# Kernel tuning notes

Measured on AMD Instinct MI355X. Metric: run time of the kernel, lower is better.

Reference implementation:

```python
import jax, jax.numpy as jnp
import numpy as np

# dims: n=batch, T=n_shifts, dX=16, dU=8, H=256 hidden, L=128 ldim, K=64 n_aux (L=2K)

def setup_inputs() -> dict:
    key = jax.random.key(0)
    ks = jax.random.split(key, 16)
    n, T, dX, dU, H, L, K = 64, 64, 16, 8, 256, 128, 64
    def lin(k, fan_in, shape):
        return (jax.random.uniform(k, shape, jnp.float32) * 2.0 - 1.0) / np.sqrt(fan_in)
    xs = jax.random.normal(ks[0], (n, T, dX), jnp.float32)
    us = jax.random.normal(ks[1], (n, T - 1, dU), jnp.float32)
    theta = jax.random.uniform(ks[2], (K,), jnp.float32) * (2.0 * np.pi)
    inp = {
        'xs': xs, 'us': us,
        # stacked x-aux encoders (K copies): BN affine, 3 linear layers (last no bias), output scale
        'x_gamma': jnp.ones((K, dX)), 'x_beta': jnp.zeros((K, dX)),
        'xW1': lin(ks[3], dX, (K, dX, H)), 'xb1': jnp.zeros((K, H)),
        'xW2': lin(ks[4], H, (K, H, H)), 'xb2': jnp.zeros((K, H)),
        'xW3': lin(ks[5], H, (K, H, L)), 'x_scale': jnp.ones((K, L)),
        # stacked u-aux encoders (K copies)
        'u_gamma': jnp.ones((K, dU)), 'u_beta': jnp.zeros((K, dU)),
        'uW1': lin(ks[6], dU, (K, dU, H)), 'ub1': jnp.zeros((K, H)),
        'uW2': lin(ks[7], H, (K, H, H)), 'ub2': jnp.zeros((K, H)),
        'uW3': lin(ks[8], H, (K, H, L)), 'u_scale': jnp.ones((K, L)),
        # Jordan-block complex eigenvalues (|lam| ~ 0.95)
        'reL': 0.95 * jnp.cos(theta), 'imL': 0.95 * jnp.sin(theta),
        # decoder C: Linear(ldim, dim, bias=False) -> weight [dX, L]
        'C_W': lin(ks[9], L, (dX, L)),
    }
    return inp


def _encoder(x, gamma, beta, W1, b1, W2, b2, W3, scale):
    # x: [M, D]; stacked params over K nets. BN stats (training mode) are per-feature over M,
    # identical across nets since the same x feeds every net.
    mu = x.mean(0)
    var = ((x - mu) ** 2).mean(0)
    xn = (x - mu) * jax.lax.rsqrt(var + 1e-5)          # [M, D]
    h = xn[None] * gamma[:, None, :] + beta[:, None, :]  # [K, M, D]
    h = jax.nn.leaky_relu(jnp.einsum('kmd,kdh->kmh', h, W1) + b1[:, None, :])
    h = jax.nn.leaky_relu(jnp.einsum('kmd,kdh->kmh', h, W2) + b2[:, None, :])
    h = jnp.einsum('kmd,kdh->kmh', h, W3)               # last layer: no bias
    return h * scale[:, None, :]                        # [K, M, L]


def reference(xs, us, x_gamma, x_beta, xW1, xb1, xW2, xb2, xW3, x_scale,
              u_gamma, u_beta, uW1, ub1, uW2, ub2, uW3, u_scale, reL, imL, C_W):
    n, T, dX = xs.shape
    K = reL.shape[0]
    L = 2 * K
    Tm1 = T - 1
    # phi1s: [n, T, K(net), K(pair), 2]
    phi = _encoder(xs.reshape(n * T, dX), x_gamma, x_beta, xW1, xb1, xW2, xb2, xW3, x_scale)
    phi1s = jnp.moveaxis(phi, 0, 1).reshape(n, T, K, K, 2)
    # ures = psi(u) - psi(0): [n, T-1, K, K, 2]
    uflat = us.reshape(n * Tm1, -1)
    psi_u = _encoder(uflat, u_gamma, u_beta, uW1, ub1, uW2, ub2, uW3, u_scale)
    psi_0 = _encoder(jnp.zeros_like(uflat), u_gamma, u_beta, uW1, ub1, uW2, ub2, uW3, u_scale)
    ures = jnp.moveaxis(psi_u - psi_0, 0, 1).reshape(n, Tm1, K, K, 2)
    # block-diagonal Koopman: per net j a 2x2 rotation-scale [[re, im], [-im, re]]
    R = jnp.stack([jnp.stack([reL, imL], -1), jnp.stack([-imL, reL], -1)], -2)  # [K, 2, 2]

    def step(p, u_t):
        p = jnp.einsum('bjkc,jcd->bjkd', p + u_t, R)
        return p, p

    _, preds = jax.lax.scan(step, phi1s[:, 0], jnp.moveaxis(ures, 0, 1))
    preds = jnp.moveaxis(preds, 0, 1)  # [n, T-1, K, K, 2]

    def phi2y(p):
        # sum over net axis (-3), flatten pair dims -> [.., L], decode with C
        return p.sum(-3).reshape(*p.shape[:-3], L) @ C_W.T

    y = phi2y(phi1s[:, 1:])
    y_pred = phi2y(preds)
    return y, y_pred
```

## Files before the change

### kernel.cpp

```cpp
#include <hip/hip_runtime.h>

typedef __bf16 bf16_t;
typedef __bf16 bf16x8 __attribute__((ext_vector_type(8)));
typedef __bf16 bf16x4 __attribute__((ext_vector_type(4)));
typedef float  f32x4  __attribute__((ext_vector_type(4)));

__global__ __launch_bounds__(256) void bn_partial_kernel(
    const float* __restrict__ xs, const float* __restrict__ us,
    float* __restrict__ part) {
    const int bid = blockIdx.x, tid = threadIdx.x;
    const bool isx = bid < 64;
    const float* x = isx ? xs : us;
    const int D   = isx ? 16 : 8;
    const int lb  = isx ? bid : bid - 64;
    const int per = isx ? (4096 * 16 / 64) : (4032 * 8 / 32);
    const int start = lb * per;
    float a = 0.f, b = 0.f;
    for (int idx = start + tid; idx < start + per; idx += 256) {
        float v = x[idx];
        a += v; b += v * v;
    }
    __shared__ float s1[256], s2[256];
    s1[tid] = a; s2[tid] = b;
    __syncthreads();
    if (tid < D) {
        float sa = 0.f, sb = 0.f;
        for (int k = tid; k < 256; k += D) { sa += s1[k]; sb += s2[k]; }
        part[bid * 32 + tid]      = sa;
        part[bid * 32 + 16 + tid] = sb;
    }
}

__global__ __launch_bounds__(64) void bn_final_kernel(
    const float* __restrict__ part, float* __restrict__ stats_x, float* __restrict__ stats_u) {
    const int tid = threadIdx.x;
    if (tid < 16) {
        float sa = 0.f, sb = 0.f;
        for (int b = 0; b < 64; b++) { sa += part[b * 32 + tid]; sb += part[b * 32 + 16 + tid]; }
        float mu = sa / 4096.f, var = sb / 4096.f - mu * mu;
        stats_x[tid] = mu; stats_x[16 + tid] = rsqrtf(var + 1e-5f);
    } else if (tid >= 32 && tid < 40) {
        const int d = tid - 32;
        float sa = 0.f, sb = 0.f;
        for (int b = 64; b < 96; b++) { sa += part[b * 32 + d]; sb += part[b * 32 + 16 + d]; }
        float mu = sa / 4032.f, var = sb / 4032.f - mu * mu;
        stats_u[d] = mu; stats_u[8 + d] = rsqrtf(var + 1e-5f);
    }
}

__global__ __launch_bounds__(256) void prep_w1_kernel(
    const float* __restrict__ xW1, const float* __restrict__ xb1,
    const float* __restrict__ xg,  const float* __restrict__ xbeta,
    const float* __restrict__ uW1, const float* __restrict__ ub1,
    const float* __restrict__ ug,  const float* __restrict__ ubeta,
    bf16_t* __restrict__ xW1t, float* __restrict__ xb1p,
    bf16_t* __restrict__ uW1t, float* __restrict__ ub1p) {
    int bid = blockIdx.x, j = bid & 63, h = threadIdx.x;
    const float *W1, *b1, *gamma, *beta; bf16_t* W1t; float* b1p; int D;
    if (bid < 64) { W1 = xW1; b1 = xb1; gamma = xg; beta = xbeta; W1t = xW1t; b1p = xb1p; D = 16; }
    else          { W1 = uW1; b1 = ub1; gamma = ug; beta = ubeta; W1t = uW1t; b1p = ub1p; D = 8; }
    float bacc = b1[j * 256 + h];
    bf16_t* orow = W1t + (size_t)(j * 256 + h) * 32;
    for (int d = 0; d < 32; d++) orow[d] = (bf16_t)0.f;
    for (int d = 0; d < D; d++) {
        float w = W1[((size_t)j * D + d) * 256 + h];
        orow[d] = (bf16_t)(gamma[j * D + d] * w);
        bacc += beta[j * D + d] * w;
    }
    b1p[j * 256 + h] = bacc;
}

__global__ __launch_bounds__(256) void transpose_all_kernel(
    const float* __restrict__ xW2, const float* __restrict__ uW2,
    const float* __restrict__ xW3, const float* __restrict__ uW3,
    const float* __restrict__ x_scale, const float* __restrict__ u_scale,
    bf16_t* __restrict__ xW2t, bf16_t* __restrict__ uW2t,
    bf16_t* __restrict__ xW3t, bf16_t* __restrict__ uW3t) {
    __shared__ float tile[32][33];
    int z = blockIdx.z, b = z & 63;
    const float* in; bf16_t* outp; const float* scale = nullptr; int C;
    if (z < 64)       { in = xW2; outp = xW2t; C = 256; }
    else if (z < 128) { in = uW2; outp = uW2t; C = 256; }
    else if (z < 192) { in = xW3; outp = xW3t; scale = x_scale + b * 128; C = 128; if (blockIdx.x >= 4) return; }
    else              { in = uW3; outp = uW3t; scale = u_scale + b * 128; C = 128; if (blockIdx.x >= 4) return; }
    const int R = 256;
    in   += (size_t)b * R * C;
    outp += (size_t)b * R * C;
    int r0 = blockIdx.y * 32, c0 = blockIdx.x * 32;
    int tx = threadIdx.x & 31, ty = threadIdx.x >> 5;
    #pragma unroll
    for (int i = 0; i < 4; i++)
        tile[ty + i * 8][tx] = in[(size_t)(r0 + ty + i * 8) * C + c0 + tx];
    __syncthreads();
    #pragma unroll
    for (int i = 0; i < 4; i++) {
        int c = c0 + ty + i * 8;
        float sc = scale ? scale[c] : 1.f;
        outp[(size_t)c * R + r0 + tx] = (bf16_t)(tile[tx][ty + i * 8] * sc);
    }
}

__global__ __launch_bounds__(512, 4) void fused_mlp_kernel(
    const float* __restrict__ xs, const float* __restrict__ us,
    const float* __restrict__ stats_x, const float* __restrict__ stats_u,
    const bf16_t* __restrict__ xW1t, const float* __restrict__ xb1p,
    const bf16_t* __restrict__ xW2t, const float* __restrict__ xb2,
    const bf16_t* __restrict__ xW3t,
    const bf16_t* __restrict__ uW1t, const float* __restrict__ ub1p,
    const bf16_t* __restrict__ uW2t, const float* __restrict__ ub2,
    const bf16_t* __restrict__ uW3t,
    bf16_t* __restrict__ phi, bf16_t* __restrict__ psiu)
{
    const int bid  = blockIdx.x;
    const int xcd  = bid & 7;
    const int slot = bid >> 3;
    const int band = slot >> 6;
    const int t64  = slot & 63;
    const int j    = xcd * 8 + band;
    const bool is_x = t64 < 32;
    const int tile  = is_x ? t64 : (t64 - 32);

    const float*  In    = is_x ? xs      : us;
    const float*  stats = is_x ? stats_x : stats_u;
    const int     D     = is_x ? 16      : 8;
    const bf16_t* W1t = is_x ? xW1t : uW1t;
    const float*  b1p = is_x ? xb1p : ub1p;
    const bf16_t* W2t = is_x ? xW2t : uW2t;
    const float*  b2  = is_x ? xb2  : ub2;
    const bf16_t* W3t = is_x ? xW3t : uW3t;
    bf16_t* outp      = is_x ? phi  : psiu;
    const int M       = is_x ? 4096 : 4032;

    const int row0 = tile * 128;
    const int tid  = threadIdx.x;
    const int wave = tid >> 6;
    const int lane = tid & 63;
    const int quad = lane >> 4;
    const int l16  = lane & 15;

    __shared__ __align__(16) bf16_t hs[128 * 256];

    const f32x4 vzero = {0.f, 0.f, 0.f, 0.f};

    {
        bf16x8 wfr[2];
        #pragma unroll
        for (int nbi = 0; nbi < 2; nbi++)
            wfr[nbi] = *reinterpret_cast<const bf16x8*>(
                W1t + (size_t)(j * 256 + wave * 32 + nbi * 16 + l16) * 32 + quad * 8);

        f32x4 acc[8][2];
        #pragma unroll
        for (int a = 0; a < 8; a++) { acc[a][0] = vzero; acc[a][1] = vzero; }

        const int c0 = quad * 8;
        #pragma unroll
        for (int mb = 0; mb < 8; mb++) {
            bf16x8 a;
            if (c0 < D) {
                int row = row0 + mb * 16 + l16;
                if (row > M - 1) row = M - 1;
                const float* xp = In + (size_t)row * D + c0;
                f32x4 v0 = *reinterpret_cast<const f32x4*>(xp);
                f32x4 v1 = *reinterpret_cast<const f32x4*>(xp + 4);
                #pragma unroll
                for (int e = 0; e < 4; e++) a[e]     = (bf16_t)((v0[e] - stats[c0 + e])     * stats[D + c0 + e]);
                #pragma unroll
                for (int e = 0; e < 4; e++) a[4 + e] = (bf16_t)((v1[e] - stats[c0 + 4 + e]) * stats[D + c0 + 4 + e]);
            } else {
                #pragma unroll
                for (int e = 0; e < 8; e++) a[e] = (bf16_t)0.f;
            }
            #pragma unroll
            for (int nbi = 0; nbi < 2; nbi++)
                acc[mb][nbi] = __builtin_amdgcn_mfma_f32_16x16x32_bf16(
                    wfr[nbi], a, acc[mb][nbi], 0, 0, 0);
        }

        #pragma unroll
        for (int nbi = 0; nbi < 2; nbi++) {
            const f32x4 bias = *reinterpret_cast<const f32x4*>(
                b1p + j * 256 + wave * 32 + nbi * 16 + quad * 4);
            const int sl = wave * 4 + nbi * 2 + (quad >> 1);
            const int half = quad & 1;
            const int sp = sl ^ l16;
            #pragma unroll
            for (int mb = 0; mb < 8; mb++) {
                const int m = mb * 16 + l16;
                bf16x4 pk;
                #pragma unroll
                for (int r = 0; r < 4; r++) {
                    float v = acc[mb][nbi][r] + bias[r];
                    v = fmaxf(v, 0.01f * v);
                    pk[r] = (bf16_t)v;
                }
                *reinterpret_cast<bf16x4*>(hs + m * 256 + sp * 8 + half * 4) = pk;
            }
        }
    }
    __syncthreads();

    {
        f32x4 acc[8][2];
        #pragma unroll
        for (int a = 0; a < 8; a++) { acc[a][0] = vzero; acc[a][1] = vzero; }

        const bf16_t* w2base = W2t + ((size_t)j * 256 + wave * 32 + l16) * 256 + quad * 8;

        bf16x8 wr[3][2];
        #pragma unroll
        for (int d = 0; d < 3; d++)
            #pragma unroll
            for (int nbi = 0; nbi < 2; nbi++)
                wr[d][nbi] = *reinterpret_cast<const bf16x8*>(w2base + nbi * 4096 + d * 32);

        #pragma unroll
        for (int kk = 0; kk < 8; kk++) {
            const int c = kk % 3;
            bf16x8 av0[4];
            #pragma unroll
            for (int mb = 0; mb < 4; mb++)
                av0[mb] = *reinterpret_cast<const bf16x8*>(
                    hs + (mb * 16 + l16) * 256 + (((kk * 4 + quad) ^ l16)) * 8);
            #pragma unroll
            for (int nbi = 0; nbi < 2; nbi++)
                #pragma unroll
                for (int mb = 0; mb < 4; mb++)
                    acc[mb][nbi] = __builtin_amdgcn_mfma_f32_16x16x32_bf16(
                        wr[c][nbi], av0[mb], acc[mb][nbi], 0, 0, 0);
            bf16x8 av1[4];
            #pragma unroll
            for (int mb = 4; mb < 8; mb++)
                av1[mb - 4] = *reinterpret_cast<const bf16x8*>(
                    hs + (mb * 16 + l16) * 256 + (((kk * 4 + quad) ^ l16)) * 8);
            #pragma unroll
            for (int nbi = 0; nbi < 2; nbi++)
                #pragma unroll
                for (int mb = 4; mb < 8; mb++)
                    acc[mb][nbi] = __builtin_amdgcn_mfma_f32_16x16x32_bf16(
                        wr[c][nbi], av1[mb - 4], acc[mb][nbi], 0, 0, 0);
            if (kk < 5) {
                #pragma unroll
                for (int nbi = 0; nbi < 2; nbi++)
                    wr[c][nbi] = *reinterpret_cast<const bf16x8*>(
                        w2base + nbi * 4096 + (kk + 3) * 32);
            }
        }
        __syncthreads();
        #pragma unroll
        for (int nbi = 0; nbi < 2; nbi++) {
            const f32x4 bias = *reinterpret_cast<const f32x4*>(
                b2 + j * 256 + wave * 32 + nbi * 16 + quad * 4);
            const int sl = wave * 4 + nbi * 2 + (quad >> 1);
            const int half = quad & 1;
            const int sp = sl ^ l16;
            #pragma unroll
            for (int mb = 0; mb < 8; mb++) {
                const int m = mb * 16 + l16;
                bf16x4 pk;
                #pragma unroll
                for (int r = 0; r < 4; r++) {
                    float v = acc[mb][nbi][r] + bias[r];
                    v = fmaxf(v, 0.01f * v);
                    pk[r] = (bf16_t)v;
                }
                *reinterpret_cast<bf16x4*>(hs + m * 256 + sp * 8 + half * 4) = pk;
            }
        }
    }
    __syncthreads();

    {
        f32x4 acc[8];
        #pragma unroll
        for (int a = 0; a < 8; a++) acc[a] = vzero;

        const bf16_t* w3base = W3t + ((size_t)j * 128 + wave * 16 + l16) * 256 + quad * 8;

        bf16x8 wr[3];
        #pragma unroll
        for (int d = 0; d < 3; d++)
            wr[d] = *reinterpret_cast<const bf16x8*>(w3base + d * 32);

        #pragma unroll
        for (int kk = 0; kk < 8; kk++) {
            const int c = kk % 3;
            bf16x8 av0[4];
            #pragma unroll
            for (int mb = 0; mb < 4; mb++)
                av0[mb] = *reinterpret_cast<const bf16x8*>(
                    hs + (mb * 16 + l16) * 256 + (((kk * 4 + quad) ^ l16)) * 8);
            #pragma unroll
            for (int mb = 0; mb < 4; mb++)
                acc[mb] = __builtin_amdgcn_mfma_f32_16x16x32_bf16(
                    wr[c], av0[mb], acc[mb], 0, 0, 0);
            bf16x8 av1[4];
            #pragma unroll
            for (int mb = 4; mb < 8; mb++)
                av1[mb - 4] = *reinterpret_cast<const bf16x8*>(
                    hs + (mb * 16 + l16) * 256 + (((kk * 4 + quad) ^ l16)) * 8);
            #pragma unroll
            for (int mb = 4; mb < 8; mb++)
                acc[mb] = __builtin_amdgcn_mfma_f32_16x16x32_bf16(
                    wr[c], av1[mb - 4], acc[mb], 0, 0, 0);
            if (kk < 5)
                wr[c] = *reinterpret_cast<const bf16x8*>(w3base + (kk + 3) * 32);
        }
        __syncthreads();
        {
            const int sl3 = wave * 2 + (quad >> 1);
            const int half = quad & 1;
            #pragma unroll
            for (int mb = 0; mb < 8; mb++) {
                const int m = mb * 16 + l16;
                const int sp = sl3 ^ l16;
                bf16x4 pk;
                #pragma unroll
                for (int r = 0; r < 4; r++) pk[r] = (bf16_t)acc[mb][r];
                *reinterpret_cast<bf16x4*>(hs + m * 128 + sp * 8 + half * 4) = pk;
            }
        }
    }
    __syncthreads();
    #pragma unroll
    for (int p = 0; p < 4; p++) {
        const int rr = p * 32 + (tid >> 4);
        const int s  = tid & 15;
        if (row0 + rr < M) {
            bf16x8 v = *reinterpret_cast<const bf16x8*>(hs + rr * 128 + (s ^ (rr & 15)) * 8);
            *reinterpret_cast<bf16x8*>(outp + ((size_t)j * M + row0 + rr) * 128 + s * 8) = v;
        }
    }
}

__global__ __launch_bounds__(256) void psi0_kernel(
    const float* __restrict__ b1p, const bf16_t* __restrict__ W2t,
    const float* __restrict__ b2, const bf16_t* __restrict__ W3t,
    float* __restrict__ psi0) {
    int j = blockIdx.x, tid = threadIdx.x;
    __shared__ float h1[256], h2[256];
    {
        float v = b1p[j * 256 + tid];
        h1[tid] = fmaxf(v, 0.01f * v);
    }
    __syncthreads();
    {
        float acc = b2[j * 256 + tid];
        const bf16_t* wrow = W2t + (size_t)(j * 256 + tid) * 256;
        for (int d = 0; d < 256; d++) acc += h1[d] * (float)wrow[d];
        h2[tid] = fmaxf(acc, 0.01f * acc);
    }
    __syncthreads();
    if (tid < 128) {
        float acc = 0.f;
        const bf16_t* wrow = W3t + (size_t)(j * 128 + tid) * 256;
        for (int d = 0; d < 256; d++) acc += h2[d] * (float)wrow[d];
        psi0[j * 128 + tid] = acc;
    }
}

__global__ __launch_bounds__(256) void y_kernel(
    const bf16_t* __restrict__ phi, const float* __restrict__ C_W,
    float* __restrict__ y) {
    const int m0 = blockIdx.x * 32;
    const int tid = threadIdx.x;
    const int r  = tid >> 3;
    const int cg = (tid & 7) * 16;
    float acc[16];
    #pragma unroll
    for (int e = 0; e < 16; e++) acc[e] = 0.f;
    const bf16_t* p = phi + (size_t)(m0 + r) * 128 + cg;
    for (int j = 0; j < 64; j++) {
        bf16x8 v0 = *reinterpret_cast<const bf16x8*>(p + (size_t)j * 524288);
        bf16x8 v1 = *reinterpret_cast<const bf16x8*>(p + (size_t)j * 524288 + 8);
        #pragma unroll
        for (int e = 0; e < 8; e++) { acc[e] += (float)v0[e]; acc[8 + e] += (float)v1[e]; }
    }
    __shared__ float S[32][128];
    #pragma unroll
    for (int e = 0; e < 16; e++) S[r][cg + e] = acc[e];
    __syncthreads();
    #pragma unroll
    for (int i = 0; i < 2; i++) {
        const int idx = tid + i * 256;
        const int mm = idx >> 4, o = idx & 15;
        const int m = m0 + mm;
        if ((m & 63) != 0) {
            float a = 0.f;
            for (int l = 0; l < 128; l++) a += S[mm][l] * C_W[o * 128 + l];
            const int b = m >> 6, ti = (m & 63) - 1;
            y[(b * 63 + ti) * 16 + o] = a;
        }
    }
}

__global__ __launch_bounds__(256) void scan_kernel(
    const bf16_t* __restrict__ phi, const bf16_t* __restrict__ psiu,
    const float* __restrict__ psi0, const float* __restrict__ reL,
    const float* __restrict__ imL, float* __restrict__ scratch) {
    const int b = blockIdx.x >> 3, jg = blockIdx.x & 7;
    const int tid = threadIdx.x;
    const int wave = tid >> 6, lane = tid & 63;
    __shared__ float red[2][4][128];

    float sx[2], sy[2], p0x[2], p0y[2], lre[2], lim[2];
    #pragma unroll
    for (int i = 0; i < 2; i++) {
        const int j = jg * 8 + wave * 2 + i;
        unsigned v = *reinterpret_cast<const unsigned*>(
            phi + ((size_t)j * 4096 + b * 64) * 128 + lane * 2);
        sx[i] = __uint_as_float(v << 16);
        sy[i] = __uint_as_float(v & 0xFFFF0000u);
        float2 p0 = *reinterpret_cast<const float2*>(psi0 + j * 128 + lane * 2);
        p0x[i] = p0.x; p0y[i] = p0.y;
        lre[i] = reL[j]; lim[i] = imL[j];
    }
    float* out = scratch + (size_t)blockIdx.x * 63 * 128;

    for (int t = 0; t < 63; t++) {
        float lsx = 0.f, lsy = 0.f;
        #pragma unroll
        for (int i = 0; i < 2; i++) {
            const int j = jg * 8 + wave * 2 + i;
            unsigned v = *reinterpret_cast<const unsigned*>(
                psiu + ((size_t)j * 4032 + b * 63 + t) * 128 + lane * 2);
            float px = sx[i] + (__uint_as_float(v << 16) - p0x[i]);
            float py = sy[i] + (__uint_as_float(v & 0xFFFF0000u) - p0y[i]);
            sx[i] = px * lre[i] - py * lim[i];
            sy[i] = px * lim[i] + py * lre[i];
            lsx += sx[i]; lsy += sy[i];
        }
        const int db = t & 1;
        red[db][wave][lane * 2]     = lsx;
        red[db][wave][lane * 2 + 1] = lsy;
        __syncthreads();
        if (tid < 128)
            out[t * 128 + tid] = red[db][0][tid] + red[db][1][tid]
                               + red[db][2][tid] + red[db][3][tid];
    }
}

__global__ __launch_bounds__(64) void decode_kernel(
    const float* __restrict__ scratch, const float* __restrict__ C_W,
    float* __restrict__ ypred) {
    const int t = blockIdx.x, b = blockIdx.y, l = threadIdx.x;
    __shared__ float S[128];
    float s0 = 0.f, s1 = 0.f;
    #pragma unroll
    for (int jg = 0; jg < 8; jg++) {
        float2 v = *reinterpret_cast<const float2*>(
            scratch + ((size_t)(b * 8 + jg) * 63 + t) * 128 + l * 2);
        s0 += v.x; s1 += v.y;
    }
    S[l * 2] = s0; S[l * 2 + 1] = s1;
    __syncthreads();
    const int o = l >> 2, q = l & 3;
    float acc = 0.f;
    #pragma unroll
    for (int i = 0; i < 32; i++)
        acc += S[q * 32 + i] * C_W[o * 128 + q * 32 + i];
    acc += __shfl_xor(acc, 2, 4);
    acc += __shfl_xor(acc, 1, 4);
    if (q == 0) ypred[(b * 63 + t) * 16 + o] = acc;
}

extern "C" void kernel_launch(void* const* d_in, const int* in_sizes, int n_in,
                              void* d_out, int out_size, void* d_ws, size_t ws_size,
                              hipStream_t stream) {
    const float* xs      = (const float*)d_in[0];
    const float* us      = (const float*)d_in[1];
    const float* x_gamma = (const float*)d_in[2];
    const float* x_beta  = (const float*)d_in[3];
    const float* xW1     = (const float*)d_in[4];
    const float* xb1     = (const float*)d_in[5];
    const float* xW2     = (const float*)d_in[6];
    const float* xb2     = (const float*)d_in[7];
    const float* xW3     = (const float*)d_in[8];
    const float* x_scale = (const float*)d_in[9];
    const float* u_gamma = (const float*)d_in[10];
    const float* u_beta  = (const float*)d_in[11];
    const float* uW1     = (const float*)d_in[12];
    const float* ub1     = (const float*)d_in[13];
    const float* uW2     = (const float*)d_in[14];
    const float* ub2     = (const float*)d_in[15];
    const float* uW3     = (const float*)d_in[16];
    const float* u_scale = (const float*)d_in[17];
    const float* reL     = (const float*)d_in[18];
    const float* imL     = (const float*)d_in[19];
    const float* C_W     = (const float*)d_in[20];

    char* ws = (char*)d_ws;
    size_t off = 0;
    auto alloc = [&](size_t bytes) -> char* {
        char* p = ws + off;
        off += (bytes + 255) & ~(size_t)255;
        return p;
    };
    float*  part    = (float*)alloc(96 * 32 * 4);
    float*  stats_x = (float*)alloc(64 * 4);
    float*  stats_u = (float*)alloc(64 * 4);
    bf16_t* xW1t = (bf16_t*)alloc((size_t)64 * 256 * 32 * 2);
    float*  xb1p = (float*) alloc((size_t)64 * 256 * 4);
    bf16_t* xW2t = (bf16_t*)alloc((size_t)64 * 256 * 256 * 2);
    bf16_t* xW3t = (bf16_t*)alloc((size_t)64 * 128 * 256 * 2);
    bf16_t* uW1t = (bf16_t*)alloc((size_t)64 * 256 * 32 * 2);
    float*  ub1p = (float*) alloc((size_t)64 * 256 * 4);
    bf16_t* uW2t = (bf16_t*)alloc((size_t)64 * 256 * 256 * 2);
    bf16_t* uW3t = (bf16_t*)alloc((size_t)64 * 128 * 256 * 2);
    float*  psi0 = (float*) alloc((size_t)64 * 128 * 4);
    bf16_t* phi  = (bf16_t*)alloc((size_t)64 * 4096 * 128 * 2);
    bf16_t* psiu = (bf16_t*)alloc((size_t)64 * 4032 * 128 * 2);
    float*  scr  = (float*) alloc((size_t)512 * 63 * 128 * 4);

    float* y_out     = (float*)d_out;
    float* ypred_out = y_out + 64 * 63 * 16;

    bn_partial_kernel<<<96, 256, 0, stream>>>(xs, us, part);
    bn_final_kernel<<<1, 64, 0, stream>>>(part, stats_x, stats_u);
    prep_w1_kernel<<<128, 256, 0, stream>>>(xW1, xb1, x_gamma, x_beta,
                                            uW1, ub1, u_gamma, u_beta,
                                            xW1t, xb1p, uW1t, ub1p);
    transpose_all_kernel<<<dim3(8, 8, 256), 256, 0, stream>>>(
        xW2, uW2, xW3, uW3, x_scale, u_scale, xW2t, uW2t, xW3t, uW3t);
    psi0_kernel<<<64, 256, 0, stream>>>(ub1p, uW2t, ub2, uW3t, psi0);
    fused_mlp_kernel<<<4096, 512, 0, stream>>>(
        xs, us, stats_x, stats_u,
        xW1t, xb1p, xW2t, xb2, xW3t, uW1t, ub1p, uW2t, ub2, uW3t, phi, psiu);
    y_kernel<<<128, 256, 0, stream>>>(phi, C_W, y_out);
    scan_kernel<<<512, 256, 0, stream>>>(phi, psiu, psi0, reL, imL, scr);
    decode_kernel<<<dim3(63, 64), 64, 0, stream>>>(scr, C_W, ypred_out);
}
```

Measured before the change: 380.3 us.

## Merge prep kernels into one launch and restructure MLP smem addressing

Five small setup kernels (BN partial sums, BN final, W1 prep, weight transposes, psi0) become one large prep launch. psi0 is now computed in fp32 from the raw weights, and the BN finalisation moves into every fused MLP block. The MLP shared-memory swizzle is rewritten with precomputed byte-offset bases, and the y kernel gets smaller tiles with C_W cached in shared memory. The scan kernel also prefetches the next psiu value one step ahead. Fewer launches and less address arithmetic are gained at the cost of redundant per-block stats reduction and a serial fp32 psi0 pass inside the prep grid.

```diff
diff --git a/kernel.cpp b/kernel.cpp
--- a/kernel.cpp
+++ b/kernel.cpp
@@ -5,104 +5,124 @@
 typedef __bf16 bf16x4 __attribute__((ext_vector_type(4)));
 typedef float  f32x4  __attribute__((ext_vector_type(4)));
 
-__global__ __launch_bounds__(256) void bn_partial_kernel(
-    const float* __restrict__ xs, const float* __restrict__ us,
-    float* __restrict__ part) {
-    const int bid = blockIdx.x, tid = threadIdx.x;
-    const bool isx = bid < 64;
-    const float* x = isx ? xs : us;
-    const int D   = isx ? 16 : 8;
-    const int lb  = isx ? bid : bid - 64;
-    const int per = isx ? (4096 * 16 / 64) : (4032 * 8 / 32);
-    const int start = lb * per;
-    float a = 0.f, b = 0.f;
-    for (int idx = start + tid; idx < start + per; idx += 256) {
-        float v = x[idx];
-        a += v; b += v * v;
-    }
-    __shared__ float s1[256], s2[256];
-    s1[tid] = a; s2[tid] = b;
-    __syncthreads();
-    if (tid < D) {
-        float sa = 0.f, sb = 0.f;
-        for (int k = tid; k < 256; k += D) { sa += s1[k]; sb += s2[k]; }
-        part[bid * 32 + tid]      = sa;
-        part[bid * 32 + 16 + tid] = sb;
-    }
-}
-
-__global__ __launch_bounds__(64) void bn_final_kernel(
-    const float* __restrict__ part, float* __restrict__ stats_x, float* __restrict__ stats_u) {
-    const int tid = threadIdx.x;
-    if (tid < 16) {
-        float sa = 0.f, sb = 0.f;
-        for (int b = 0; b < 64; b++) { sa += part[b * 32 + tid]; sb += part[b * 32 + 16 + tid]; }
-        float mu = sa / 4096.f, var = sb / 4096.f - mu * mu;
-        stats_x[tid] = mu; stats_x[16 + tid] = rsqrtf(var + 1e-5f);
-    } else if (tid >= 32 && tid < 40) {
-        const int d = tid - 32;
-        float sa = 0.f, sb = 0.f;
-        for (int b = 64; b < 96; b++) { sa += part[b * 32 + d]; sb += part[b * 32 + 16 + d]; }
-        float mu = sa / 4032.f, var = sb / 4032.f - mu * mu;
-        stats_u[d] = mu; stats_u[8 + d] = rsqrtf(var + 1e-5f);
-    }
-}
-
-__global__ __launch_bounds__(256) void prep_w1_kernel(
+__global__ __launch_bounds__(256) void prep_all_kernel(
     const float* __restrict__ xW1, const float* __restrict__ xb1,
     const float* __restrict__ xg,  const float* __restrict__ xbeta,
     const float* __restrict__ uW1, const float* __restrict__ ub1,
     const float* __restrict__ ug,  const float* __restrict__ ubeta,
-    bf16_t* __restrict__ xW1t, float* __restrict__ xb1p,
-    bf16_t* __restrict__ uW1t, float* __restrict__ ub1p) {
-    int bid = blockIdx.x, j = bid & 63, h = threadIdx.x;
-    const float *W1, *b1, *gamma, *beta; bf16_t* W1t; float* b1p; int D;
-    if (bid < 64) { W1 = xW1; b1 = xb1; gamma = xg; beta = xbeta; W1t = xW1t; b1p = xb1p; D = 16; }
-    else          { W1 = uW1; b1 = ub1; gamma = ug; beta = ubeta; W1t = uW1t; b1p = ub1p; D = 8; }
-    float bacc = b1[j * 256 + h];
-    bf16_t* orow = W1t + (size_t)(j * 256 + h) * 32;
-    for (int d = 0; d < 32; d++) orow[d] = (bf16_t)0.f;
-    for (int d = 0; d < D; d++) {
-        float w = W1[((size_t)j * D + d) * 256 + h];
-        orow[d] = (bf16_t)(gamma[j * D + d] * w);
-        bacc += beta[j * D + d] * w;
-    }
-    b1p[j * 256 + h] = bacc;
-}
-
-__global__ __launch_bounds__(256) void transpose_all_kernel(
     const float* __restrict__ xW2, const float* __restrict__ uW2,
     const float* __restrict__ xW3, const float* __restrict__ uW3,
     const float* __restrict__ x_scale, const float* __restrict__ u_scale,
+    const float* __restrict__ ub2,
+    const float* __restrict__ xs, const float* __restrict__ us,
+    bf16_t* __restrict__ xW1t, float* __restrict__ xb1p,
+    bf16_t* __restrict__ uW1t, float* __restrict__ ub1p,
     bf16_t* __restrict__ xW2t, bf16_t* __restrict__ uW2t,
-    bf16_t* __restrict__ xW3t, bf16_t* __restrict__ uW3t) {
+    bf16_t* __restrict__ xW3t, bf16_t* __restrict__ uW3t,
+    float* __restrict__ psi0, float* __restrict__ part)
+{
+    const int t = blockIdx.x, tid = threadIdx.x;
     __shared__ float tile[32][33];
-    int z = blockIdx.z, b = z & 63;
-    const float* in; bf16_t* outp; const float* scale = nullptr; int C;
-    if (z < 64)       { in = xW2; outp = xW2t; C = 256; }
-    else if (z < 128) { in = uW2; outp = uW2t; C = 256; }
-    else if (z < 192) { in = xW3; outp = xW3t; scale = x_scale + b * 128; C = 128; if (blockIdx.x >= 4) return; }
-    else              { in = uW3; outp = uW3t; scale = u_scale + b * 128; C = 128; if (blockIdx.x >= 4) return; }
-    const int R = 256;
-    in   += (size_t)b * R * C;
-    outp += (size_t)b * R * C;
-    int r0 = blockIdx.y * 32, c0 = blockIdx.x * 32;
-    int tx = threadIdx.x & 31, ty = threadIdx.x >> 5;
-    #pragma unroll
-    for (int i = 0; i < 4; i++)
-        tile[ty + i * 8][tx] = in[(size_t)(r0 + ty + i * 8) * C + c0 + tx];
-    __syncthreads();
-    #pragma unroll
-    for (int i = 0; i < 4; i++) {
-        int c = c0 + ty + i * 8;
-        float sc = scale ? scale[c] : 1.f;
-        outp[(size_t)c * R + r0 + tx] = (bf16_t)(tile[tx][ty + i * 8] * sc);
+    __shared__ float h1[256], h2[256];
+
+    if (t < 12288) {
+        const float* in; bf16_t* outp; const float* scale = nullptr;
+        int j, r0, c0, C;
+        if (t < 8192) {
+            C = 256;
+            j = (t & 4095) >> 6;
+            const int tl = t & 63; r0 = (tl >> 3) * 32; c0 = (tl & 7) * 32;
+            if (t < 4096) { in = xW2; outp = xW2t; }
+            else          { in = uW2; outp = uW2t; }
+        } else {
+            C = 128;
+            const int l = t - 8192;
+            j = (l & 2047) >> 5;
+            const int tl = l & 31; r0 = (tl >> 2) * 32; c0 = (tl & 3) * 32;
+            if (l < 2048) { in = xW3; outp = xW3t; scale = x_scale + j * 128; }
+            else          { in = uW3; outp = uW3t; scale = u_scale + j * 128; }
+        }
+        const int R = 256;
+        in   += (size_t)j * R * C;
+        bf16_t* op = outp + (size_t)j * R * C;
+        const int tx = tid & 31, ty = tid >> 5;
+        #pragma unroll
+        for (int i = 0; i < 4; i++)
+            tile[ty + i * 8][tx] = in[(size_t)(r0 + ty + i * 8) * C + c0 + tx];
+        __syncthreads();
+        #pragma unroll
+        for (int i = 0; i < 4; i++) {
+            int c = c0 + ty + i * 8;
+            float sc = scale ? scale[c] : 1.f;
+            op[(size_t)c * R + r0 + tx] = (bf16_t)(tile[tx][ty + i * 8] * sc);
+        }
+    } else if (t < 12416) {
+        const int bid = t - 12288, j = bid & 63, h = tid;
+        const float *W1, *b1, *gamma, *beta; bf16_t* W1t; float* b1p; int D;
+        if (bid < 64) { W1 = xW1; b1 = xb1; gamma = xg; beta = xbeta; W1t = xW1t; b1p = xb1p; D = 16; }
+        else          { W1 = uW1; b1 = ub1; gamma = ug; beta = ubeta; W1t = uW1t; b1p = ub1p; D = 8; }
+        float bacc = b1[j * 256 + h];
+        bf16_t* orow = W1t + (size_t)(j * 256 + h) * 32;
+        for (int d = 0; d < 32; d++) orow[d] = (bf16_t)0.f;
+        for (int d = 0; d < D; d++) {
+            float w = W1[((size_t)j * D + d) * 256 + h];
+            orow[d] = (bf16_t)(gamma[j * D + d] * w);
+            bacc += beta[j * D + d] * w;
+        }
+        b1p[j * 256 + h] = bacc;
+    } else if (t < 12480) {
+        const int j = t - 12416, h = tid;
+        {
+            float bacc = ub1[j * 256 + h];
+            #pragma unroll
+            for (int d = 0; d < 8; d++)
+                bacc += ubeta[j * 8 + d] * uW1[((size_t)j * 8 + d) * 256 + h];
+            h1[h] = fmaxf(bacc, 0.01f * bacc);
+        }
+        __syncthreads();
+        {
+            float acc = ub2[j * 256 + h];
+            const float* w2 = uW2 + (size_t)j * 65536 + h;
+            #pragma unroll 8
+            for (int d = 0; d < 256; d++) acc += h1[d] * w2[d * 256];
+            h2[h] = fmaxf(acc, 0.01f * acc);
+        }
+        __syncthreads();
+        if (h < 128) {
+            float acc = 0.f;
+            const float* w3 = uW3 + (size_t)j * 32768 + h;
+            #pragma unroll 8
+            for (int d = 0; d < 256; d++) acc += h2[d] * w3[d * 128];
+            psi0[j * 128 + h] = acc * u_scale[j * 128 + h];
+        }
+    } else {
+        const int bid = t - 12480;
+        const bool isx = bid < 64;
+        const float* x = isx ? xs : us;
+        const int D   = isx ? 16 : 8;
+        const int lb  = isx ? bid : bid - 64;
+        const int per = isx ? 1024 : 1008;
+        const int start = lb * per;
+        float a = 0.f, b = 0.f;
+        for (int idx = start + tid; idx < start + per; idx += 256) {
+            float v = x[idx];
+            a += v; b += v * v;
+        }
+        float* s1 = h1; float* s2 = h2;
+        s1[tid] = a; s2[tid] = b;
+        __syncthreads();
+        if (tid < D) {
+            float sa = 0.f, sb = 0.f;
+            for (int k = tid; k < 256; k += D) { sa += s1[k]; sb += s2[k]; }
+            part[bid * 32 + tid]      = sa;
+            part[bid * 32 + 16 + tid] = sb;
+        }
     }
 }
 
 __global__ __launch_bounds__(512, 4) void fused_mlp_kernel(
     const float* __restrict__ xs, const float* __restrict__ us,
-    const float* __restrict__ stats_x, const float* __restrict__ stats_u,
+    const float* __restrict__ part,
     const bf16_t* __restrict__ xW1t, const float* __restrict__ xb1p,
     const bf16_t* __restrict__ xW2t, const float* __restrict__ xb2,
     const bf16_t* __restrict__ xW3t,
@@ -120,9 +140,8 @@
     const bool is_x = t64 < 32;
     const int tile  = is_x ? t64 : (t64 - 32);
 
-    const float*  In    = is_x ? xs      : us;
-    const float*  stats = is_x ? stats_x : stats_u;
-    const int     D     = is_x ? 16      : 8;
+    const float*  In  = is_x ? xs   : us;
+    const int     D   = is_x ? 16   : 8;
     const bf16_t* W1t = is_x ? xW1t : uW1t;
     const float*  b1p = is_x ? xb1p : ub1p;
     const bf16_t* W2t = is_x ? xW2t : uW2t;
@@ -137,10 +156,34 @@
     const int lane = tid & 63;
     const int quad = lane >> 4;
     const int l16  = lane & 15;
+    const int lo2  = l16 & 3, hi2 = l16 >> 2;
 
     __shared__ __align__(16) bf16_t hs[128 * 256];
+    __shared__ float stats_s[32];
+
+    if (tid < 16) {
+        if (is_x) {
+            float sa = 0.f, sb = 0.f;
+            #pragma unroll 8
+            for (int b = 0; b < 64; b++) { sa += part[b * 32 + tid]; sb += part[b * 32 + 16 + tid]; }
+            float mu = sa / 4096.f, var = sb / 4096.f - mu * mu;
+            stats_s[tid] = mu; stats_s[16 + tid] = rsqrtf(var + 1e-5f);
+        } else if (tid < 8) {
+            float sa = 0.f, sb = 0.f;
+            #pragma unroll 8
+            for (int b = 64; b < 96; b++) { sa += part[b * 32 + tid]; sb += part[b * 32 + 16 + tid]; }
+            float mu = sa / 4032.f, var = sb / 4032.f - mu * mu;
+            stats_s[tid] = mu; stats_s[16 + tid] = rsqrtf(var + 1e-5f);
+        }
+    }
+    __syncthreads();
 
     const f32x4 vzero = {0.f, 0.f, 0.f, 0.f};
+
+    char* const hsB = (char*)hs;
+    const char* const abase = hsB + l16 * 512 + ((quad ^ lo2) << 4);
+    const int  wlow0 = (quad >> 1) ^ lo2;
+    char* const wbase = hsB + l16 * 512 + ((wave ^ hi2) << 6) + ((quad & 1) << 3);
 
     {
         bf16x8 wfr[2];
@@ -164,9 +207,9 @@
                 f32x4 v0 = *reinterpret_cast<const f32x4*>(xp);
                 f32x4 v1 = *reinterpret_cast<const f32x4*>(xp + 4);
                 #pragma unroll
-                for (int e = 0; e < 4; e++) a[e]     = (bf16_t)((v0[e] - stats[c0 + e])     * stats[D + c0 + e]);
-                #pragma unroll
-                for (int e = 0; e < 4; e++) a[4 + e] = (bf16_t)((v1[e] - stats[c0 + 4 + e]) * stats[D + c0 + 4 + e]);
+                for (int e = 0; e < 4; e++) a[e]     = (bf16_t)((v0[e] - stats_s[c0 + e])     * stats_s[16 + c0 + e]);
+                #pragma unroll
+                for (int e = 0; e < 4; e++) a[4 + e] = (bf16_t)((v1[e] - stats_s[c0 + 4 + e]) * stats_s[16 + c0 + 4 + e]);
             } else {
                 #pragma unroll
                 for (int e = 0; e < 8; e++) a[e] = (bf16_t)0.f;
@@ -181,12 +224,9 @@
         for (int nbi = 0; nbi < 2; nbi++) {
             const f32x4 bias = *reinterpret_cast<const f32x4*>(
                 b1p + j * 256 + wave * 32 + nbi * 16 + quad * 4);
-            const int sl = wave * 4 + nbi * 2 + (quad >> 1);
-            const int half = quad & 1;
-            const int sp = sl ^ l16;
+            char* wp = wbase + ((wlow0 ^ (nbi << 1)) << 4);
             #pragma unroll
             for (int mb = 0; mb < 8; mb++) {
-                const int m = mb * 16 + l16;
                 bf16x4 pk;
                 #pragma unroll
                 for (int r = 0; r < 4; r++) {
@@ -194,7 +234,7 @@
                     v = fmaxf(v, 0.01f * v);
                     pk[r] = (bf16_t)v;
                 }
-                *reinterpret_cast<bf16x4*>(hs + m * 256 + sp * 8 + half * 4) = pk;
+                *reinterpret_cast<bf16x4*>(wp + mb * 8192) = pk;
             }
         }
     }
@@ -217,11 +257,11 @@
         #pragma unroll
         for (int kk = 0; kk < 8; kk++) {
             const int c = kk % 3;
+            const char* ap = abase + ((kk ^ hi2) << 6);
             bf16x8 av0[4];
             #pragma unroll
             for (int mb = 0; mb < 4; mb++)
-                av0[mb] = *reinterpret_cast<const bf16x8*>(
-                    hs + (mb * 16 + l16) * 256 + (((kk * 4 + quad) ^ l16)) * 8);
+                av0[mb] = *reinterpret_cast<const bf16x8*>(ap + mb * 8192);
             #pragma unroll
             for (int nbi = 0; nbi < 2; nbi++)
                 #pragma unroll
@@ -230,9 +270,8 @@
                         wr[c][nbi], av0[mb], acc[mb][nbi], 0, 0, 0);
             bf16x8 av1[4];
             #pragma unroll
-            for (int mb = 4; mb < 8; mb++)
-                av1[mb - 4] = *reinterpret_cast<const bf16x8*>(
-                    hs + (mb * 16 + l16) * 256 + (((kk * 4 + quad) ^ l16)) * 8);
+            for (int mb = 0; mb < 4; mb++)
+                av1[mb] = *reinterpret_cast<const bf16x8*>(ap + (mb + 4) * 8192);
             #pragma unroll
             for (int nbi = 0; nbi < 2; nbi++)
                 #pragma unroll
@@ -251,12 +290,9 @@
         for (int nbi = 0; nbi < 2; nbi++) {
             const f32x4 bias = *reinterpret_cast<const f32x4*>(
                 b2 + j * 256 + wave * 32 + nbi * 16 + quad * 4);
-            const int sl = wave * 4 + nbi * 2 + (quad >> 1);
-            const int half = quad & 1;
-            const int sp = sl ^ l16;
+            char* wp = wbase + ((wlow0 ^ (nbi << 1)) << 4);
             #pragma unroll
             for (int mb = 0; mb < 8; mb++) {
-                const int m = mb * 16 + l16;
                 bf16x4 pk;
                 #pragma unroll
                 for (int r = 0; r < 4; r++) {
@@ -264,7 +300,7 @@
                     v = fmaxf(v, 0.01f * v);
                     pk[r] = (bf16_t)v;
                 }
-                *reinterpret_cast<bf16x4*>(hs + m * 256 + sp * 8 + half * 4) = pk;
+                *reinterpret_cast<bf16x4*>(wp + mb * 8192) = pk;
             }
         }
     }
@@ -285,20 +321,19 @@
         #pragma unroll
         for (int kk = 0; kk < 8; kk++) {
             const int c = kk % 3;
+            const char* ap = abase + ((kk ^ hi2) << 6);
             bf16x8 av0[4];
             #pragma unroll
             for (int mb = 0; mb < 4; mb++)
-                av0[mb] = *reinterpret_cast<const bf16x8*>(
-                    hs + (mb * 16 + l16) * 256 + (((kk * 4 + quad) ^ l16)) * 8);
+                av0[mb] = *reinterpret_cast<const bf16x8*>(ap + mb * 8192);
             #pragma unroll
             for (int mb = 0; mb < 4; mb++)
                 acc[mb] = __builtin_amdgcn_mfma_f32_16x16x32_bf16(
                     wr[c], av0[mb], acc[mb], 0, 0, 0);
             bf16x8 av1[4];
             #pragma unroll
-            for (int mb = 4; mb < 8; mb++)
-                av1[mb - 4] = *reinterpret_cast<const bf16x8*>(
-                    hs + (mb * 16 + l16) * 256 + (((kk * 4 + quad) ^ l16)) * 8);
+            for (int mb = 0; mb < 4; mb++)
+                av1[mb] = *reinterpret_cast<const bf16x8*>(ap + (mb + 4) * 8192);
             #pragma unroll
             for (int mb = 4; mb < 8; mb++)
                 acc[mb] = __builtin_amdgcn_mfma_f32_16x16x32_bf16(
@@ -308,16 +343,14 @@
         }
         __syncthreads();
         {
-            const int sl3 = wave * 2 + (quad >> 1);
-            const int half = quad & 1;
+            const int sp3 = (wave * 2 + (quad >> 1)) ^ l16;
+            char* w3p = hsB + l16 * 256 + sp3 * 16 + ((quad & 1) << 3);
             #pragma unroll
             for (int mb = 0; mb < 8; mb++) {
-                const int m = mb * 16 + l16;
-                const int sp = sl3 ^ l16;
                 bf16x4 pk;
                 #pragma unroll
                 for (int r = 0; r < 4; r++) pk[r] = (bf16_t)acc[mb][r];
-                *reinterpret_cast<bf16x4*>(hs + m * 128 + sp * 8 + half * 4) = pk;
+                *reinterpret_cast<bf16x4*>(w3p + mb * 4096) = pk;
             }
         }
     }
@@ -333,64 +366,37 @@
     }
 }
 
-__global__ __launch_bounds__(256) void psi0_kernel(
-    const float* __restrict__ b1p, const bf16_t* __restrict__ W2t,
-    const float* __restrict__ b2, const bf16_t* __restrict__ W3t,
-    float* __restrict__ psi0) {
-    int j = blockIdx.x, tid = threadIdx.x;
-    __shared__ float h1[256], h2[256];
-    {
-        float v = b1p[j * 256 + tid];
-        h1[tid] = fmaxf(v, 0.01f * v);
-    }
-    __syncthreads();
-    {
-        float acc = b2[j * 256 + tid];
-        const bf16_t* wrow = W2t + (size_t)(j * 256 + tid) * 256;
-        for (int d = 0; d < 256; d++) acc += h1[d] * (float)wrow[d];
-        h2[tid] = fmaxf(acc, 0.01f * acc);
-    }
-    __syncthreads();
-    if (tid < 128) {
-        float acc = 0.f;
-        const bf16_t* wrow = W3t + (size_t)(j * 128 + tid) * 256;
-        for (int d = 0; d < 256; d++) acc += h2[d] * (float)wrow[d];
-        psi0[j * 128 + tid] = acc;
-    }
-}
-
 __global__ __launch_bounds__(256) void y_kernel(
     const bf16_t* __restrict__ phi, const float* __restrict__ C_W,
     float* __restrict__ y) {
-    const int m0 = blockIdx.x * 32;
+    const int m0 = blockIdx.x * 16;
     const int tid = threadIdx.x;
-    const int r  = tid >> 3;
-    const int cg = (tid & 7) * 16;
-    float acc[16];
+    __shared__ float S[16][128];
+    __shared__ float Cs[2048];
     #pragma unroll
-    for (int e = 0; e < 16; e++) acc[e] = 0.f;
+    for (int i = 0; i < 8; i++) Cs[tid + i * 256] = C_W[tid + i * 256];
+    const int r  = tid >> 4;
+    const int cg = (tid & 15) * 8;
+    float acc[8];
+    #pragma unroll
+    for (int e = 0; e < 8; e++) acc[e] = 0.f;
     const bf16_t* p = phi + (size_t)(m0 + r) * 128 + cg;
     for (int j = 0; j < 64; j++) {
-        bf16x8 v0 = *reinterpret_cast<const bf16x8*>(p + (size_t)j * 524288);
-        bf16x8 v1 = *reinterpret_cast<const bf16x8*>(p + (size_t)j * 524288 + 8);
-        #pragma unroll
-        for (int e = 0; e < 8; e++) { acc[e] += (float)v0[e]; acc[8 + e] += (float)v1[e]; }
-    }
-    __shared__ float S[32][128];
+        bf16x8 v = *reinterpret_cast<const bf16x8*>(p + (size_t)j * 524288);
+        #pragma unroll
+        for (int e = 0; e < 8; e++) acc[e] += (float)v[e];
+    }
     #pragma unroll
-    for (int e = 0; e < 16; e++) S[r][cg + e] = acc[e];
+    for (int e = 0; e < 8; e++) S[r][cg + e] = acc[e];
     __syncthreads();
-    #pragma unroll
-    for (int i = 0; i < 2; i++) {
-        const int idx = tid + i * 256;
-        const int mm = idx >> 4, o = idx & 15;
-        const int m = m0 + mm;
-        if ((m & 63) != 0) {
-            float a = 0.f;
-            for (int l = 0; l < 128; l++) a += S[mm][l] * C_W[o * 128 + l];
-            const int b = m >> 6, ti = (m & 63) - 1;
-            y[(b * 63 + ti) * 16 + o] = a;
-        }
+    const int mm = tid >> 4, o = tid & 15;
+    const int m = m0 + mm;
+    if ((m & 63) != 0) {
+        float a = 0.f;
+        #pragma unroll 8
+        for (int l = 0; l < 128; l++) a += S[mm][l] * Cs[o * 128 + l];
+        const int b = m >> 6, ti = (m & 63) - 1;
+        y[(b * 63 + ti) * 16 + o] = a;
     }
 }
 
@@ -403,40 +409,49 @@
     const int wave = tid >> 6, lane = tid & 63;
     __shared__ float red[2][4][128];
 
-    float sx[2], sy[2], p0x[2], p0y[2], lre[2], lim[2];
-    #pragma unroll
-    for (int i = 0; i < 2; i++) {
-        const int j = jg * 8 + wave * 2 + i;
-        unsigned v = *reinterpret_cast<const unsigned*>(
-            phi + ((size_t)j * 4096 + b * 64) * 128 + lane * 2);
-        sx[i] = __uint_as_float(v << 16);
-        sy[i] = __uint_as_float(v & 0xFFFF0000u);
-        float2 p0 = *reinterpret_cast<const float2*>(psi0 + j * 128 + lane * 2);
-        p0x[i] = p0.x; p0y[i] = p0.y;
-        lre[i] = reL[j]; lim[i] = imL[j];
-    }
+    const int j0 = jg * 8 + wave * 2;
+    float sx0, sy0, sx1, sy1;
+    float p0x0, p0y0, p0x1, p0y1, lre0, lim0, lre1, lim1;
+    {
+        unsigned v0 = *reinterpret_cast<const unsigned*>(
+            phi + ((size_t)j0 * 4096 + b * 64) * 128 + lane * 2);
+        unsigned v1 = *reinterpret_cast<const unsigned*>(
+            phi + ((size_t)(j0 + 1) * 4096 + b * 64) * 128 + lane * 2);
+        sx0 = __uint_as_float(v0 << 16); sy0 = __uint_as_float(v0 & 0xFFFF0000u);
+        sx1 = __uint_as_float(v1 << 16); sy1 = __uint_as_float(v1 & 0xFFFF0000u);
+        float2 p0 = *reinterpret_cast<const float2*>(psi0 + j0 * 128 + lane * 2);
+        float2 p1 = *reinterpret_cast<const float2*>(psi0 + (j0 + 1) * 128 + lane * 2);
+        p0x0 = p0.x; p0y0 = p0.y; p0x1 = p1.x; p0y1 = p1.y;
+        lre0 = reL[j0]; lim0 = imL[j0]; lre1 = reL[j0 + 1]; lim1 = imL[j0 + 1];
+    }
+    const bf16_t* up0 = psiu + ((size_t)j0 * 4032 + b * 63) * 128 + lane * 2;
+    const bf16_t* up1 = psiu + ((size_t)(j0 + 1) * 4032 + b * 63) * 128 + lane * 2;
+    unsigned cur0 = *reinterpret_cast<const unsigned*>(up0);
+    unsigned cur1 = *reinterpret_cast<const unsigned*>(up1);
     float* out = scratch + (size_t)blockIdx.x * 63 * 128;
 
     for (int t = 0; t < 63; t++) {
-        float lsx = 0.f, lsy = 0.f;
-        #pragma unroll
-        for (int i = 0; i < 2; i++) {
-            const int j = jg * 8 + wave * 2 + i;
-            unsigned v = *reinterpret_cast<const unsigned*>(
-                psiu + ((size_t)j * 4032 + b * 63 + t) * 128 + lane * 2);
-            float px = sx[i] + (__uint_as_float(v << 16) - p0x[i]);
-            float py = sy[i] + (__uint_as_float(v & 0xFFFF0000u) - p0y[i]);
-            sx[i] = px * lre[i] - py * lim[i];
-            sy[i] = px * lim[i] + py * lre[i];
-            lsx += sx[i]; lsy += sy[i];
-        }
+        unsigned nx0 = 0, nx1 = 0;
+        if (t < 62) {
+            nx0 = *reinterpret_cast<const unsigned*>(up0 + (t + 1) * 128);
+            nx1 = *reinterpret_cast<const unsigned*>(up1 + (t + 1) * 128);
+        }
+        float px = sx0 + (__uint_as_float(cur0 << 16) - p0x0);
+        float py = sy0 + (__uint_as_float(cur0 & 0xFFFF0000u) - p0y0);
+        sx0 = px * lre0 - py * lim0;
+        sy0 = px * lim0 + py * lre0;
+        px = sx1 + (__uint_as_float(cur1 << 16) - p0x1);
+        py = sy1 + (__uint_as_float(cur1 & 0xFFFF0000u) - p0y1);
+        sx1 = px * lre1 - py * lim1;
+        sy1 = px * lim1 + py * lre1;
         const int db = t & 1;
-        red[db][wave][lane * 2]     = lsx;
-        red[db][wave][lane * 2 + 1] = lsy;
+        red[db][wave][lane * 2]     = sx0 + sx1;
+        red[db][wave][lane * 2 + 1] = sy0 + sy1;
         __syncthreads();
         if (tid < 128)
             out[t * 128 + tid] = red[db][0][tid] + red[db][1][tid]
                                + red[db][2][tid] + red[db][3][tid];
+        cur0 = nx0; cur1 = nx1;
     }
 }
 
@@ -496,9 +511,7 @@
         off += (bytes + 255) & ~(size_t)255;
         return p;
     };
-    float*  part    = (float*)alloc(96 * 32 * 4);
-    float*  stats_x = (float*)alloc(64 * 4);
-    float*  stats_u = (float*)alloc(64 * 4);
+    float*  part = (float*)alloc(96 * 32 * 4);
     bf16_t* xW1t = (bf16_t*)alloc((size_t)64 * 256 * 32 * 2);
     float*  xb1p = (float*) alloc((size_t)64 * 256 * 4);
     bf16_t* xW2t = (bf16_t*)alloc((size_t)64 * 256 * 256 * 2);
@@ -515,18 +528,14 @@
     float* y_out     = (float*)d_out;
     float* ypred_out = y_out + 64 * 63 * 16;
 
-    bn_partial_kernel<<<96, 256, 0, stream>>>(xs, us, part);
-    bn_final_kernel<<<1, 64, 0, stream>>>(part, stats_x, stats_u);
-    prep_w1_kernel<<<128, 256, 0, stream>>>(xW1, xb1, x_gamma, x_beta,
-                                            uW1, ub1, u_gamma, u_beta,
-                                            xW1t, xb1p, uW1t, ub1p);
-    transpose_all_kernel<<<dim3(8, 8, 256), 256, 0, stream>>>(
-        xW2, uW2, xW3, uW3, x_scale, u_scale, xW2t, uW2t, xW3t, uW3t);
-    psi0_kernel<<<64, 256, 0, stream>>>(ub1p, uW2t, ub2, uW3t, psi0);
+    prep_all_kernel<<<12576, 256, 0, stream>>>(
+        xW1, xb1, x_gamma, x_beta, uW1, ub1, u_gamma, u_beta,
+        xW2, uW2, xW3, uW3, x_scale, u_scale, ub2, xs, us,
+        xW1t, xb1p, uW1t, ub1p, xW2t, uW2t, xW3t, uW3t, psi0, part);
     fused_mlp_kernel<<<4096, 512, 0, stream>>>(
-        xs, us, stats_x, stats_u,
+        xs, us, part,
         xW1t, xb1p, xW2t, xb2, xW3t, uW1t, ub1p, uW2t, ub2, uW3t, phi, psiu);
-    y_kernel<<<128, 256, 0, stream>>>(phi, C_W, y_out);
+    y_kernel<<<256, 256, 0, stream>>>(phi, C_W, y_out);
     scan_kernel<<<512, 256, 0, stream>>>(phi, psiu, psi0, reL, imL, scr);
     decode_kernel<<<dim3(63, 64), 64, 0, stream>>>(scr, C_W, ypred_out);
 }
```

Result: faster. 362.7 us, median of 2 (-4.6%).
